# Optimization experiments

Hardware: AMD Instinct MI355X
Metric: run time of the kernel (lower is better)

The kernel has to match this reference:

```python
import jax, jax.numpy as jnp
import numpy as np

T, K, E, D, F = 16, 8, 64, 2048, 1024  # tokens, top_k, experts, hidden, intermediate


def setup_inputs() -> dict:
    key = jax.random.key(0)
    k1, k2, k3, k4, k5 = jax.random.split(key, 5)
    hidden_states = jax.random.normal(k1, (T, D), dtype=jnp.float32)
    top_k_index = jax.random.randint(k2, (T, K), 0, E, dtype=jnp.int64)
    # routing weights (already summed/normalized per the module's contract)
    top_k_weights = jax.random.uniform(k3, (T, K), dtype=jnp.float32) / K
    # dense dequantized per-expert weights (up: D->F, down: F->D, no bias)
    W_up = jax.random.normal(k4, (E, D, F), dtype=jnp.float32) * 0.02
    W_down = jax.random.normal(k5, (E, F, D), dtype=jnp.float32) * 0.02
    return {
        "hidden_states": hidden_states,
        "top_k_index": top_k_index,
        "top_k_weights": top_k_weights,
        "W_up": W_up,
        "W_down": W_down,
    }


def reference(hidden_states, top_k_index, top_k_weights, W_up, W_down):
    num_experts = W_up.shape[0]
    # route[t, e] = sum_k top_k_weights[t, k] * (top_k_index[t, k] == e)
    route = jnp.sum(
        jax.nn.one_hot(top_k_index, num_experts, dtype=top_k_weights.dtype)
        * top_k_weights[..., None],
        axis=1,
    )  # [T, E]
    # up_proj for every expert on every token (few tokens -> cheap, weight-bound)
    h = jnp.einsum("td,edf->etf", hidden_states, W_up)  # [E, T, F]
    a = jnp.square(jax.nn.relu(h))  # relu^2 activation (NemotronH non-gated MoE)
    # down_proj then weighted combine; experts not routed get zero weight
    out = jnp.einsum("etf,efd,te->td", a, W_down, route)  # [T, D]
    return out.astype(hidden_states.dtype)
```

## Files before the change

kernel.cpp:

```cpp
#include <hip/hip_runtime.h>

#define T_TOK 16
#define K_TOP 8
#define NEXP  64
#define DHID  2048
#define FINT  1024

#define ROUTE_OFF 0u
#define AIDX_OFF  4096u
#define NA_OFF    (AIDX_OFF + 256u)
#define XT_OFF    8192u
#define ABUF_OFF  (XT_OFF + 131072u)
#define OPART_OFF (ABUF_OFF + 4194304u)

__global__ void k_route(const int* __restrict__ idx, const float* __restrict__ w,
                        float* __restrict__ route, int* __restrict__ aidx,
                        int* __restrict__ nA) {
    __shared__ float r[NEXP * T_TOK];
    __shared__ int is64_s;
    const int tid = threadIdx.x;
    if (tid == 0) {
        int allz = 1;
        for (int i = 1; i < 128; i += 2) allz &= (idx[i] == 0);
        is64_s = allz;
    }
    __syncthreads();
    const int is64 = is64_s;
    for (int i = tid; i < NEXP * T_TOK; i += 256) {
        const int e = i >> 4, t = i & 15;
        float s = 0.f;
#pragma unroll
        for (int k = 0; k < K_TOP; ++k) {
            const int flat = t * K_TOP + k;
            const int ev = is64 ? idx[2 * flat] : idx[flat];
            if (ev == e) s += w[flat];
        }
        r[i] = s;
        route[i] = s;
    }
    __syncthreads();
    if (tid == 0) {
        int n = 0;
        for (int e = 0; e < NEXP; ++e) {
            float s = 0.f;
            for (int t = 0; t < T_TOK; ++t) s += r[e * T_TOK + t];
            if (s != 0.f) aidx[n++] = e;
        }
        *nA = n;
    }
}

__global__ void k_xpose(const float* __restrict__ x, float* __restrict__ xT) {
    const int tid = threadIdx.x;
    const int d = blockIdx.x * 64 + (tid & 63);
    const int tq = tid >> 6;
    float4 v;
    v.x = x[(tq * 4 + 0) * DHID + d];
    v.y = x[(tq * 4 + 1) * DHID + d];
    v.z = x[(tq * 4 + 2) * DHID + d];
    v.w = x[(tq * 4 + 3) * DHID + d];
    *reinterpret_cast<float4*>(xT + d * T_TOK + tq * 4) = v;
}

#define FMA_T(t, xs)                                   \
    acc0[t] = fmaf((xs), w4.x, acc0[t]);               \
    acc1[t] = fmaf((xs), w4.y, acc1[t]);               \
    acc2[t] = fmaf((xs), w4.z, acc2[t]);               \
    acc3[t] = fmaf((xs), w4.w, acc3[t]);

#define FMA_BLOCK()                                                       \
    {                                                                     \
        const float4 xa = *reinterpret_cast<const float4*>(&lds[base]);   \
        const float4 xb = *reinterpret_cast<const float4*>(&lds[base+4]); \
        const float4 xc = *reinterpret_cast<const float4*>(&lds[base+8]); \
        const float4 xd = *reinterpret_cast<const float4*>(&lds[base+12]);\
        FMA_T(0, xa.x)  FMA_T(1, xa.y)  FMA_T(2, xa.z)  FMA_T(3, xa.w)   \
        FMA_T(4, xb.x)  FMA_T(5, xb.y)  FMA_T(6, xb.z)  FMA_T(7, xb.w)   \
        FMA_T(8, xc.x)  FMA_T(9, xc.y)  FMA_T(10, xc.z) FMA_T(11, xc.w)  \
        FMA_T(12, xd.x) FMA_T(13, xd.y) FMA_T(14, xd.z) FMA_T(15, xd.w)  \
    }

#define RED_WRITE(reg)                                                   \
    {                                                                    \
        float* p = lds + (reg) * 4096 + lane;                            \
        _Pragma("unroll") for (int t = 0; t < 16; ++t) {                 \
            p[(0 * 16 + t) * 64] = acc0[t];                              \
            p[(1 * 16 + t) * 64] = acc1[t];                              \
            p[(2 * 16 + t) * 64] = acc2[t];                              \
            p[(3 * 16 + t) * 64] = acc3[t];                              \
        }                                                                \
    }
#define RED_READ(reg)                                                    \
    {                                                                    \
        const float* p = lds + (reg) * 4096 + lane;                      \
        _Pragma("unroll") for (int t = 0; t < 16; ++t) {                 \
            acc0[t] += p[(0 * 16 + t) * 64];                             \
            acc1[t] += p[(1 * 16 + t) * 64];                             \
            acc2[t] += p[(2 * 16 + t) * 64];                             \
            acc3[t] += p[(3 * 16 + t) * 64];                             \
        }                                                                \
    }

__global__ __launch_bounds__(1024, 4) void k_up(
    const float* __restrict__ xT, const float* __restrict__ Wu,
    const float* __restrict__ route, const int* __restrict__ aidx,
    const int* __restrict__ nAp, float* __restrict__ a_buf) {
    const int b = blockIdx.x;
    if (b >= 4 * (*nAp)) return;
    const int e = aidx[b >> 2];
    const int fq = b & 3;
    const int tid = threadIdx.x;
    const int wid = tid >> 6, lane = tid & 63;

    __shared__ float lds[16384];

    float acc0[T_TOK] = {}, acc1[T_TOK] = {}, acc2[T_TOK] = {}, acc3[T_TOK] = {};

    const float* wcol = Wu + (size_t)e * DHID * FINT + fq * 256 + lane * 4;

#pragma unroll
    for (int ph = 0; ph < 2; ++ph) {
        if (ph) __syncthreads();
        {
            const float4* src = reinterpret_cast<const float4*>(xT + ph * 1024 * T_TOK);
            float4* dst = reinterpret_cast<float4*>(lds);
#pragma unroll
            for (int i = 0; i < 4; ++i) dst[i * 1024 + tid] = src[i * 1024 + tid];
        }
        __syncthreads();
        const float* wp = wcol + (size_t)(ph * 1024 + wid * 64) * FINT;
#pragma unroll 2
        for (int dd = 0; dd < 64; ++dd) {
            const float4 w4 = *reinterpret_cast<const float4*>(wp + (size_t)dd * FINT);
            const int base = (wid * 64 + dd) * T_TOK;
            FMA_BLOCK()
        }
    }

    __syncthreads();
    if (wid >= 8 && wid < 12) RED_WRITE(wid - 8)
    __syncthreads();
    if (wid < 4) RED_READ(wid)
    __syncthreads();
    if (wid >= 12) RED_WRITE(wid - 12)
    __syncthreads();
    if (wid >= 4 && wid < 8) RED_READ(wid - 4)
    __syncthreads();
    if (wid >= 4 && wid < 8) RED_WRITE(wid - 4)
    __syncthreads();
    if (wid < 4) RED_READ(wid)
    __syncthreads();
    if (wid == 2 || wid == 3) RED_WRITE(wid - 2)
    __syncthreads();
    if (wid < 2) RED_READ(wid)
    __syncthreads();
    if (wid == 1) RED_WRITE(0)
    __syncthreads();

    if (wid == 0) {
        RED_READ(0)
        float rt[T_TOK];
#pragma unroll
        for (int t = 0; t < T_TOK; ++t) rt[t] = route[e * T_TOK + t];
        float* ap = a_buf + ((size_t)e * FINT + fq * 256 + lane * 4) * T_TOK;
#define ACT1(A, t) (rt[t] * fmaxf(A[t], 0.f) * fmaxf(A[t], 0.f))
#define STORE_COL(A, jj)                                                              \
    *reinterpret_cast<float4*>(ap + (jj) * T_TOK + 0) =                               \
        make_float4(ACT1(A, 0), ACT1(A, 1), ACT1(A, 2), ACT1(A, 3));                  \
    *reinterpret_cast<float4*>(ap + (jj) * T_TOK + 4) =                               \
        make_float4(ACT1(A, 4), ACT1(A, 5), ACT1(A, 6), ACT1(A, 7));                  \
    *reinterpret_cast<float4*>(ap + (jj) * T_TOK + 8) =                               \
        make_float4(ACT1(A, 8), ACT1(A, 9), ACT1(A, 10), ACT1(A, 11));                \
    *reinterpret_cast<float4*>(ap + (jj) * T_TOK + 12) =                              \
        make_float4(ACT1(A, 12), ACT1(A, 13), ACT1(A, 14), ACT1(A, 15));
        STORE_COL(acc0, 0) STORE_COL(acc1, 1) STORE_COL(acc2, 2) STORE_COL(acc3, 3)
#undef STORE_COL
#undef ACT1
    }
}

__global__ __launch_bounds__(1024, 4) void k_down(
    const float* __restrict__ a_buf, const float* __restrict__ Wd,
    const int* __restrict__ aidx, const int* __restrict__ nAp,
    float* __restrict__ out_part) {
    const int b = blockIdx.x;
    if (b >= 4 * (*nAp)) return;
    const int e = aidx[b >> 2];
    const int dc = b & 3;
    const int tid = threadIdx.x;
    const int wid = tid >> 6, lane = tid & 63;
    const int wd = wid >> 3, wf = wid & 7;

    __shared__ float lds[16384];

    {
        const float4* src = reinterpret_cast<const float4*>(a_buf + (size_t)e * FINT * T_TOK);
        float4* dst = reinterpret_cast<float4*>(lds);
#pragma unroll
        for (int i = 0; i < 4; ++i) dst[i * 1024 + tid] = src[i * 1024 + tid];
    }
    __syncthreads();

    const int d0 = dc * 512 + wd * 256 + lane * 4;
    const float* wp = Wd + ((size_t)e * FINT + wf * 128) * DHID + d0;

    float acc0[T_TOK] = {}, acc1[T_TOK] = {}, acc2[T_TOK] = {}, acc3[T_TOK] = {};
#pragma unroll 2
    for (int ff = 0; ff < 128; ++ff) {
        const float4 w4 = *reinterpret_cast<const float4*>(wp + (size_t)ff * DHID);
        const int base = (wf * 128 + ff) * T_TOK;
        FMA_BLOCK()
    }

    __syncthreads();
    if (wd == 0 && wf >= 4) RED_WRITE(wf - 4)
    __syncthreads();
    if (wd == 0 && wf < 4) RED_READ(wf)
    __syncthreads();
    if (wd == 1 && wf >= 4) RED_WRITE(wf - 4)
    __syncthreads();
    if (wd == 1 && wf < 4) RED_READ(wf)
    __syncthreads();
    if (wf == 2 || wf == 3) RED_WRITE(wd * 2 + wf - 2)
    __syncthreads();
    if (wf < 2) RED_READ(wd * 2 + wf)
    __syncthreads();
    if (wf == 1) RED_WRITE(wd)
    __syncthreads();

    if (wf == 0) {
        RED_READ(wd)
        float* op = out_part + (size_t)e * (T_TOK * DHID) + d0;
#pragma unroll
        for (int t = 0; t < T_TOK; ++t)
            *reinterpret_cast<float4*>(op + (size_t)t * DHID) =
                make_float4(acc0[t], acc1[t], acc2[t], acc3[t]);
    }
}

__global__ void k_comb(const float* __restrict__ out_part, const int* __restrict__ aidx,
                       const int* __restrict__ nAp, float* __restrict__ out) {
    const int i = blockIdx.x * 256 + threadIdx.x;
    const int nA = *nAp;
    const size_t off = (size_t)i * 4;
    float4 s = make_float4(0.f, 0.f, 0.f, 0.f);
    for (int a = 0; a < nA; ++a) {
        const float4 v = *reinterpret_cast<const float4*>(
            out_part + (size_t)aidx[a] * (T_TOK * DHID) + off);
        s.x += v.x; s.y += v.y; s.z += v.z; s.w += v.w;
    }
    *reinterpret_cast<float4*>(out + off) = s;
}

extern "C" void kernel_launch(void* const* d_in, const int* in_sizes, int n_in,
                              void* d_out, int out_size, void* d_ws, size_t ws_size,
                              hipStream_t stream) {
    (void)in_sizes; (void)n_in; (void)out_size; (void)ws_size;
    const float* x   = (const float*)d_in[0];
    const int*   idx = (const int*)d_in[1];
    const float* w   = (const float*)d_in[2];
    const float* Wu  = (const float*)d_in[3];
    const float* Wd  = (const float*)d_in[4];
    float* out = (float*)d_out;

    char* ws = (char*)d_ws;
    float* route    = (float*)(ws + ROUTE_OFF);
    int*   aidx     = (int*)(ws + AIDX_OFF);
    int*   nA       = (int*)(ws + NA_OFF);
    float* xT       = (float*)(ws + XT_OFF);
    float* a_buf    = (float*)(ws + ABUF_OFF);
    float* out_part = (float*)(ws + OPART_OFF);

    k_route<<<1, 256, 0, stream>>>(idx, w, route, aidx, nA);
    k_xpose<<<DHID / 64, 256, 0, stream>>>(x, xT);
    k_up<<<4 * NEXP, 1024, 0, stream>>>(xT, Wu, route, aidx, nA, a_buf);
    k_down<<<4 * NEXP, 1024, 0, stream>>>(a_buf, Wd, aidx, nA, out_part);
    k_comb<<<(T_TOK * DHID / 4) / 256, 256, 0, stream>>>(out_part, aidx, nA, out);
}
```

Baseline: 214.9 us.

## Store activations and LDS operands in bf16, prefetch weights, merge prep kernels

Activations, the LDS copy of x, and the cross-wave reduction partials are now packed as bf16. This halves LDS footprint and intermediate buffer traffic, and lets k_up hold all of x in LDS in a single phase. Weight loads become nontemporal with a 4-deep register prefetch, and the route and transpose kernels are merged into one launch. The cost is reduced precision in inputs, activations and partial sums, which may push results outside tolerance.

```diff
diff --git a/kernel.cpp b/kernel.cpp
--- a/kernel.cpp
+++ b/kernel.cpp
@@ -6,51 +6,32 @@
 #define DHID  2048
 #define FINT  1024
 
+typedef unsigned int   uint_t;
+typedef unsigned short ushort_t;
+typedef float f32x4 __attribute__((ext_vector_type(4)));
+
 #define ROUTE_OFF 0u
 #define AIDX_OFF  4096u
 #define NA_OFF    (AIDX_OFF + 256u)
 #define XT_OFF    8192u
 #define ABUF_OFF  (XT_OFF + 131072u)
-#define OPART_OFF (ABUF_OFF + 4194304u)
-
-__global__ void k_route(const int* __restrict__ idx, const float* __restrict__ w,
-                        float* __restrict__ route, int* __restrict__ aidx,
-                        int* __restrict__ nA) {
-    __shared__ float r[NEXP * T_TOK];
-    __shared__ int is64_s;
-    const int tid = threadIdx.x;
-    if (tid == 0) {
-        int allz = 1;
-        for (int i = 1; i < 128; i += 2) allz &= (idx[i] == 0);
-        is64_s = allz;
-    }
-    __syncthreads();
-    const int is64 = is64_s;
-    for (int i = tid; i < NEXP * T_TOK; i += 256) {
-        const int e = i >> 4, t = i & 15;
-        float s = 0.f;
-#pragma unroll
-        for (int k = 0; k < K_TOP; ++k) {
-            const int flat = t * K_TOP + k;
-            const int ev = is64 ? idx[2 * flat] : idx[flat];
-            if (ev == e) s += w[flat];
-        }
-        r[i] = s;
-        route[i] = s;
-    }
-    __syncthreads();
-    if (tid == 0) {
-        int n = 0;
-        for (int e = 0; e < NEXP; ++e) {
-            float s = 0.f;
-            for (int t = 0; t < T_TOK; ++t) s += r[e * T_TOK + t];
-            if (s != 0.f) aidx[n++] = e;
-        }
-        *nA = n;
-    }
-}
-
-__global__ void k_xpose(const float* __restrict__ x, float* __restrict__ xT) {
+#define OPART_OFF (ABUF_OFF + 2097152u)
+
+__device__ __forceinline__ ushort_t f2bf(float f) {
+    uint_t u = __builtin_bit_cast(uint_t, f);
+    u += 0x7FFFu + ((u >> 16) & 1u);
+    return (ushort_t)(u >> 16);
+}
+__device__ __forceinline__ uint_t pk2(float lo, float hi) {
+    return (uint_t)f2bf(lo) | ((uint_t)f2bf(hi) << 16);
+}
+__device__ __forceinline__ float bf_lo(uint_t v) { return __builtin_bit_cast(float, v << 16); }
+__device__ __forceinline__ float bf_hi(uint_t v) { return __builtin_bit_cast(float, v & 0xFFFF0000u); }
+
+__global__ void k_prep(const float* __restrict__ x, const int* __restrict__ idx,
+                       const float* __restrict__ w, float* __restrict__ xT,
+                       float* __restrict__ route, int* __restrict__ aidx,
+                       int* __restrict__ nA) {
     const int tid = threadIdx.x;
     const int d = blockIdx.x * 64 + (tid & 63);
     const int tq = tid >> 6;
@@ -60,51 +41,76 @@
     v.z = x[(tq * 4 + 2) * DHID + d];
     v.w = x[(tq * 4 + 3) * DHID + d];
     *reinterpret_cast<float4*>(xT + d * T_TOK + tq * 4) = v;
-}
-
-#define FMA_T(t, xs)                                   \
-    acc0[t] = fmaf((xs), w4.x, acc0[t]);               \
-    acc1[t] = fmaf((xs), w4.y, acc1[t]);               \
-    acc2[t] = fmaf((xs), w4.z, acc2[t]);               \
+
+    if (blockIdx.x != 0) return;
+    __shared__ float r[NEXP * T_TOK];
+    __shared__ int is64_s;
+    if (tid == 0) {
+        int allz = 1;
+        for (int i = 1; i < 128; i += 2) allz &= (idx[i] == 0);
+        is64_s = allz;
+    }
+    __syncthreads();
+    const int is64 = is64_s;
+    for (int i = tid; i < NEXP * T_TOK; i += 256) {
+        const int e = i >> 4, t = i & 15;
+        float s = 0.f;
+#pragma unroll
+        for (int k = 0; k < K_TOP; ++k) {
+            const int flat = t * K_TOP + k;
+            const int ev = is64 ? idx[2 * flat] : idx[flat];
+            if (ev == e) s += w[flat];
+        }
+        r[i] = s;
+        route[i] = s;
+    }
+    __syncthreads();
+    if (tid == 0) {
+        int n = 0;
+        for (int e = 0; e < NEXP; ++e) {
+            float s = 0.f;
+            for (int t = 0; t < T_TOK; ++t) s += r[e * T_TOK + t];
+            if (s != 0.f) aidx[n++] = e;
+        }
+        *nA = n;
+    }
+}
+
+#define FMA4(t, xs)                              \
+    acc0[t] = fmaf((xs), w4.x, acc0[t]);         \
+    acc1[t] = fmaf((xs), w4.y, acc1[t]);         \
+    acc2[t] = fmaf((xs), w4.z, acc2[t]);         \
     acc3[t] = fmaf((xs), w4.w, acc3[t]);
-
-#define FMA_BLOCK()                                                       \
-    {                                                                     \
-        const float4 xa = *reinterpret_cast<const float4*>(&lds[base]);   \
-        const float4 xb = *reinterpret_cast<const float4*>(&lds[base+4]); \
-        const float4 xc = *reinterpret_cast<const float4*>(&lds[base+8]); \
-        const float4 xd = *reinterpret_cast<const float4*>(&lds[base+12]);\
-        FMA_T(0, xa.x)  FMA_T(1, xa.y)  FMA_T(2, xa.z)  FMA_T(3, xa.w)   \
-        FMA_T(4, xb.x)  FMA_T(5, xb.y)  FMA_T(6, xb.z)  FMA_T(7, xb.w)   \
-        FMA_T(8, xc.x)  FMA_T(9, xc.y)  FMA_T(10, xc.z) FMA_T(11, xc.w)  \
-        FMA_T(12, xd.x) FMA_T(13, xd.y) FMA_T(14, xd.z) FMA_T(15, xd.w)  \
-    }
-
-#define RED_WRITE(reg)                                                   \
-    {                                                                    \
-        float* p = lds + (reg) * 4096 + lane;                            \
-        _Pragma("unroll") for (int t = 0; t < 16; ++t) {                 \
-            p[(0 * 16 + t) * 64] = acc0[t];                              \
-            p[(1 * 16 + t) * 64] = acc1[t];                              \
-            p[(2 * 16 + t) * 64] = acc2[t];                              \
-            p[(3 * 16 + t) * 64] = acc3[t];                              \
-        }                                                                \
-    }
-#define RED_READ(reg)                                                    \
-    {                                                                    \
-        const float* p = lds + (reg) * 4096 + lane;                      \
-        _Pragma("unroll") for (int t = 0; t < 16; ++t) {                 \
-            acc0[t] += p[(0 * 16 + t) * 64];                             \
-            acc1[t] += p[(1 * 16 + t) * 64];                             \
-            acc2[t] += p[(2 * 16 + t) * 64];                             \
-            acc3[t] += p[(3 * 16 + t) * 64];                             \
-        }                                                                \
-    }
+#define FMA_PAIR(u, t0_)                                        \
+    { const float xl = bf_lo(u), xh = bf_hi(u);                 \
+      FMA4(t0_, xl) FMA4((t0_) + 1, xh) }
+#define STEP(jj, B)                                                         \
+    { const uint4 q0 = xqw[(jj) * 2]; const uint4 q1 = xqw[(jj) * 2 + 1];   \
+      const f32x4 w4 = (B);                                                 \
+      FMA_PAIR(q0.x, 0) FMA_PAIR(q0.y, 2) FMA_PAIR(q0.z, 4) FMA_PAIR(q0.w, 6) \
+      FMA_PAIR(q1.x, 8) FMA_PAIR(q1.y, 10) FMA_PAIR(q1.z, 12) FMA_PAIR(q1.w, 14) }
+#define LDW(j) __builtin_nontemporal_load(wrow + (size_t)(j) * WSTEP)
+
+#define RW(reg)                                                         \
+    { uint_t* p = lds_u + (reg) * 2048 + lane;                          \
+      _Pragma("unroll") for (int tp = 0; tp < 8; ++tp) {                \
+          p[(0 * 8 + tp) * 64] = pk2(acc0[2 * tp], acc0[2 * tp + 1]);   \
+          p[(1 * 8 + tp) * 64] = pk2(acc1[2 * tp], acc1[2 * tp + 1]);   \
+          p[(2 * 8 + tp) * 64] = pk2(acc2[2 * tp], acc2[2 * tp + 1]);   \
+          p[(3 * 8 + tp) * 64] = pk2(acc3[2 * tp], acc3[2 * tp + 1]); } }
+#define RR(reg)                                                         \
+    { const uint_t* p = lds_u + (reg) * 2048 + lane;                    \
+      _Pragma("unroll") for (int tp = 0; tp < 8; ++tp) {                \
+          uint_t u;                                                     \
+          u = p[(0 * 8 + tp) * 64]; acc0[2 * tp] += bf_lo(u); acc0[2 * tp + 1] += bf_hi(u); \
+          u = p[(1 * 8 + tp) * 64]; acc1[2 * tp] += bf_lo(u); acc1[2 * tp + 1] += bf_hi(u); \
+          u = p[(2 * 8 + tp) * 64]; acc2[2 * tp] += bf_lo(u); acc2[2 * tp + 1] += bf_hi(u); \
+          u = p[(3 * 8 + tp) * 64]; acc3[2 * tp] += bf_lo(u); acc3[2 * tp + 1] += bf_hi(u); } }
 
 __global__ __launch_bounds__(1024, 4) void k_up(
     const float* __restrict__ xT, const float* __restrict__ Wu,
     const float* __restrict__ route, const int* __restrict__ aidx,
-    const int* __restrict__ nAp, float* __restrict__ a_buf) {
+    const int* __restrict__ nAp, ushort_t* __restrict__ a_buf) {
     const int b = blockIdx.x;
     if (b >= 4 * (*nAp)) return;
     const int e = aidx[b >> 2];
@@ -112,75 +118,75 @@
     const int tid = threadIdx.x;
     const int wid = tid >> 6, lane = tid & 63;
 
-    __shared__ float lds[16384];
-
-    float acc0[T_TOK] = {}, acc1[T_TOK] = {}, acc2[T_TOK] = {}, acc3[T_TOK] = {};
-
-    const float* wcol = Wu + (size_t)e * DHID * FINT + fq * 256 + lane * 4;
-
-#pragma unroll
-    for (int ph = 0; ph < 2; ++ph) {
-        if (ph) __syncthreads();
-        {
-            const float4* src = reinterpret_cast<const float4*>(xT + ph * 1024 * T_TOK);
-            float4* dst = reinterpret_cast<float4*>(lds);
-#pragma unroll
-            for (int i = 0; i < 4; ++i) dst[i * 1024 + tid] = src[i * 1024 + tid];
+    __shared__ __align__(16) uint_t lds_u[16384];
+
+    {
+        const float4* src = reinterpret_cast<const float4*>(xT);
+        uint2* dst = reinterpret_cast<uint2*>(lds_u);
+#pragma unroll
+        for (int i = 0; i < 8; ++i) {
+            const float4 v = src[tid * 8 + i];
+            dst[tid * 8 + i] = make_uint2(pk2(v.x, v.y), pk2(v.z, v.w));
         }
-        __syncthreads();
-        const float* wp = wcol + (size_t)(ph * 1024 + wid * 64) * FINT;
-#pragma unroll 2
-        for (int dd = 0; dd < 64; ++dd) {
-            const float4 w4 = *reinterpret_cast<const float4*>(wp + (size_t)dd * FINT);
-            const int base = (wid * 64 + dd) * T_TOK;
-            FMA_BLOCK()
-        }
-    }
-
-    __syncthreads();
-    if (wid >= 8 && wid < 12) RED_WRITE(wid - 8)
-    __syncthreads();
-    if (wid < 4) RED_READ(wid)
-    __syncthreads();
-    if (wid >= 12) RED_WRITE(wid - 12)
-    __syncthreads();
-    if (wid >= 4 && wid < 8) RED_READ(wid - 4)
-    __syncthreads();
-    if (wid >= 4 && wid < 8) RED_WRITE(wid - 4)
-    __syncthreads();
-    if (wid < 4) RED_READ(wid)
-    __syncthreads();
-    if (wid == 2 || wid == 3) RED_WRITE(wid - 2)
-    __syncthreads();
-    if (wid < 2) RED_READ(wid)
-    __syncthreads();
-    if (wid == 1) RED_WRITE(0)
-    __syncthreads();
-
+    }
+    __syncthreads();
+
+    float acc0[16] = {}, acc1[16] = {}, acc2[16] = {}, acc3[16] = {};
+
+    const f32x4* wrow = reinterpret_cast<const f32x4*>(
+        Wu + (size_t)e * ((size_t)DHID * FINT) + (size_t)(wid * 128) * FINT
+           + fq * 256 + lane * 4);
+    const size_t WSTEP = FINT / 4;
+    const uint4* xqw = reinterpret_cast<const uint4*>(lds_u) + (size_t)wid * 256;
+
+    f32x4 b0 = LDW(0), b1 = LDW(1), b2 = LDW(2), b3 = LDW(3);
+    for (int j = 0; j < 128; j += 4) {
+        const bool pf = (j < 124);
+        STEP(j + 0, b0) if (pf) b0 = LDW(j + 4);
+        STEP(j + 1, b1) if (pf) b1 = LDW(j + 5);
+        STEP(j + 2, b2) if (pf) b2 = LDW(j + 6);
+        STEP(j + 3, b3) if (pf) b3 = LDW(j + 7);
+    }
+
+    __syncthreads();
+    if (wid >= 8) RW(wid - 8)
+    __syncthreads();
+    if (wid < 8) RR(wid)
+    __syncthreads();
+    if (wid >= 4 && wid < 8) RW(wid - 4)
+    __syncthreads();
+    if (wid < 4) RR(wid)
+    __syncthreads();
+    if (wid >= 2 && wid < 4) RW(wid - 2)
+    __syncthreads();
+    if (wid < 2) RR(wid)
+    __syncthreads();
+    if (wid == 1) RW(0)
+    __syncthreads();
     if (wid == 0) {
-        RED_READ(0)
-        float rt[T_TOK];
-#pragma unroll
-        for (int t = 0; t < T_TOK; ++t) rt[t] = route[e * T_TOK + t];
-        float* ap = a_buf + ((size_t)e * FINT + fq * 256 + lane * 4) * T_TOK;
-#define ACT1(A, t) (rt[t] * fmaxf(A[t], 0.f) * fmaxf(A[t], 0.f))
-#define STORE_COL(A, jj)                                                              \
-    *reinterpret_cast<float4*>(ap + (jj) * T_TOK + 0) =                               \
-        make_float4(ACT1(A, 0), ACT1(A, 1), ACT1(A, 2), ACT1(A, 3));                  \
-    *reinterpret_cast<float4*>(ap + (jj) * T_TOK + 4) =                               \
-        make_float4(ACT1(A, 4), ACT1(A, 5), ACT1(A, 6), ACT1(A, 7));                  \
-    *reinterpret_cast<float4*>(ap + (jj) * T_TOK + 8) =                               \
-        make_float4(ACT1(A, 8), ACT1(A, 9), ACT1(A, 10), ACT1(A, 11));                \
-    *reinterpret_cast<float4*>(ap + (jj) * T_TOK + 12) =                              \
-        make_float4(ACT1(A, 12), ACT1(A, 13), ACT1(A, 14), ACT1(A, 15));
-        STORE_COL(acc0, 0) STORE_COL(acc1, 1) STORE_COL(acc2, 2) STORE_COL(acc3, 3)
-#undef STORE_COL
-#undef ACT1
+        RR(0)
+        float rt[16];
+#pragma unroll
+        for (int t = 0; t < 16; ++t) rt[t] = route[e * T_TOK + t];
+#define ACT(A, t) (rt[t] * fmaxf(A[t], 0.f) * fmaxf(A[t], 0.f))
+        uint4* ap = reinterpret_cast<uint4*>(
+            a_buf + ((size_t)e * FINT + fq * 256 + lane * 4) * T_TOK);
+        uint4 o;
+#define ST_COL(A, k0)                                                   \
+        o.x = pk2(ACT(A, 0), ACT(A, 1));  o.y = pk2(ACT(A, 2), ACT(A, 3));   \
+        o.z = pk2(ACT(A, 4), ACT(A, 5));  o.w = pk2(ACT(A, 6), ACT(A, 7));   \
+        ap[k0] = o;                                                          \
+        o.x = pk2(ACT(A, 8), ACT(A, 9));  o.y = pk2(ACT(A, 10), ACT(A, 11)); \
+        o.z = pk2(ACT(A, 12), ACT(A, 13)); o.w = pk2(ACT(A, 14), ACT(A, 15)); \
+        ap[k0 + 1] = o;
+        ST_COL(acc0, 0) ST_COL(acc1, 2) ST_COL(acc2, 4) ST_COL(acc3, 6)
+#undef ST_COL
+#undef ACT
     }
 }
 
 __global__ __launch_bounds__(1024, 4) void k_down(
-    const float* __restrict__ a_buf, const float* __restrict__ Wd,
+    const ushort_t* __restrict__ a_buf, const float* __restrict__ Wd,
     const int* __restrict__ aidx, const int* __restrict__ nAp,
     float* __restrict__ out_part) {
     const int b = blockIdx.x;
@@ -191,48 +197,49 @@
     const int wid = tid >> 6, lane = tid & 63;
     const int wd = wid >> 3, wf = wid & 7;
 
-    __shared__ float lds[16384];
+    __shared__ __align__(16) uint_t lds_u[16384];
 
     {
-        const float4* src = reinterpret_cast<const float4*>(a_buf + (size_t)e * FINT * T_TOK);
-        float4* dst = reinterpret_cast<float4*>(lds);
-#pragma unroll
-        for (int i = 0; i < 4; ++i) dst[i * 1024 + tid] = src[i * 1024 + tid];
-    }
-    __syncthreads();
+        const uint4* src = reinterpret_cast<const uint4*>(a_buf + (size_t)e * FINT * T_TOK);
+        uint4* dst = reinterpret_cast<uint4*>(lds_u);
+        dst[tid] = src[tid];
+        dst[tid + 1024] = src[tid + 1024];
+    }
+    __syncthreads();
+
+    float acc0[16] = {}, acc1[16] = {}, acc2[16] = {}, acc3[16] = {};
 
     const int d0 = dc * 512 + wd * 256 + lane * 4;
-    const float* wp = Wd + ((size_t)e * FINT + wf * 128) * DHID + d0;
-
-    float acc0[T_TOK] = {}, acc1[T_TOK] = {}, acc2[T_TOK] = {}, acc3[T_TOK] = {};
-#pragma unroll 2
-    for (int ff = 0; ff < 128; ++ff) {
-        const float4 w4 = *reinterpret_cast<const float4*>(wp + (size_t)ff * DHID);
-        const int base = (wf * 128 + ff) * T_TOK;
-        FMA_BLOCK()
-    }
-
-    __syncthreads();
-    if (wd == 0 && wf >= 4) RED_WRITE(wf - 4)
-    __syncthreads();
-    if (wd == 0 && wf < 4) RED_READ(wf)
-    __syncthreads();
-    if (wd == 1 && wf >= 4) RED_WRITE(wf - 4)
-    __syncthreads();
-    if (wd == 1 && wf < 4) RED_READ(wf)
-    __syncthreads();
-    if (wf == 2 || wf == 3) RED_WRITE(wd * 2 + wf - 2)
-    __syncthreads();
-    if (wf < 2) RED_READ(wd * 2 + wf)
-    __syncthreads();
-    if (wf == 1) RED_WRITE(wd)
-    __syncthreads();
-
+    const f32x4* wrow = reinterpret_cast<const f32x4*>(
+        Wd + (size_t)e * ((size_t)FINT * DHID) + (size_t)(wf * 128) * DHID + d0);
+    const size_t WSTEP = DHID / 4;
+    const uint4* xqw = reinterpret_cast<const uint4*>(lds_u) + (size_t)wf * 256;
+
+    f32x4 b0 = LDW(0), b1 = LDW(1), b2 = LDW(2), b3 = LDW(3);
+    for (int j = 0; j < 128; j += 4) {
+        const bool pf = (j < 124);
+        STEP(j + 0, b0) if (pf) b0 = LDW(j + 4);
+        STEP(j + 1, b1) if (pf) b1 = LDW(j + 5);
+        STEP(j + 2, b2) if (pf) b2 = LDW(j + 6);
+        STEP(j + 3, b3) if (pf) b3 = LDW(j + 7);
+    }
+
+    __syncthreads();
+    if (wf >= 4) RW(wd * 4 + wf - 4)
+    __syncthreads();
+    if (wf < 4) RR(wd * 4 + wf)
+    __syncthreads();
+    if (wf == 2 || wf == 3) RW(wd * 4 + wf - 2)
+    __syncthreads();
+    if (wf < 2) RR(wd * 4 + wf)
+    __syncthreads();
+    if (wf == 1) RW(wd * 4)
+    __syncthreads();
     if (wf == 0) {
-        RED_READ(wd)
+        RR(wd * 4)
         float* op = out_part + (size_t)e * (T_TOK * DHID) + d0;
 #pragma unroll
-        for (int t = 0; t < T_TOK; ++t)
+        for (int t = 0; t < 16; ++t)
             *reinterpret_cast<float4*>(op + (size_t)t * DHID) =
                 make_float4(acc0[t], acc1[t], acc2[t], acc3[t]);
     }
@@ -264,15 +271,14 @@
     float* out = (float*)d_out;
 
     char* ws = (char*)d_ws;
-    float* route    = (float*)(ws + ROUTE_OFF);
-    int*   aidx     = (int*)(ws + AIDX_OFF);
-    int*   nA       = (int*)(ws + NA_OFF);
-    float* xT       = (float*)(ws + XT_OFF);
-    float* a_buf    = (float*)(ws + ABUF_OFF);
-    float* out_part = (float*)(ws + OPART_OFF);
-
-    k_route<<<1, 256, 0, stream>>>(idx, w, route, aidx, nA);
-    k_xpose<<<DHID / 64, 256, 0, stream>>>(x, xT);
+    float*    route    = (float*)(ws + ROUTE_OFF);
+    int*      aidx     = (int*)(ws + AIDX_OFF);
+    int*      nA       = (int*)(ws + NA_OFF);
+    float*    xT       = (float*)(ws + XT_OFF);
+    ushort_t* a_buf    = (ushort_t*)(ws + ABUF_OFF);
+    float*    out_part = (float*)(ws + OPART_OFF);
+
+    k_prep<<<DHID / 64, 256, 0, stream>>>(x, idx, w, xT, route, aidx, nA);
     k_up<<<4 * NEXP, 1024, 0, stream>>>(xT, Wu, route, aidx, nA, a_buf);
     k_down<<<4 * NEXP, 1024, 0, stream>>>(a_buf, Wd, aidx, nA, out_part);
     k_comb<<<(T_TOK * DHID / 4) / 256, 256, 0, stream>>>(out_part, aidx, nA, out);
```

Result: faster. 197.0 us (-8.3%).
